# Performance work log

Hardware: AMD Instinct MI355X
Metric: run time of the kernel (lower is better)

Reference implementation:

```python
import jax, jax.numpy as jnp
import numpy as np

N, IN_F, OUT_F, R = 8192, 4096, 4096, 16
ALPHA = 32
SCALING = ALPHA / R  # 2.0


def setup_inputs() -> dict:
    key = jax.random.key(0)
    k1, k2, k3, k4, k5 = jax.random.split(key, 5)
    return {
        "x": jax.random.normal(k1, (N, IN_F), dtype=jnp.float32),
        "W": jax.random.normal(k2, (OUT_F, IN_F), dtype=jnp.float32) * 0.02,
        "b": jax.random.normal(k3, (OUT_F,), dtype=jnp.float32) * 0.02,
        "lora_A": jax.random.normal(k4, (R, IN_F), dtype=jnp.float32) * 0.02,
        "lora_B": jax.random.normal(k5, (OUT_F, R), dtype=jnp.float32) * 0.02,
    }


def reference(x, W, b, lora_A, lora_B):
    # Base linear: x [N, in_f] @ W.T [in_f, out_f] + b -> [N, out_f]
    result = jnp.einsum('ni,oi->no', x, W) + b
    # LoRA path: (B @ (A @ x.T)).T * scaling == (x @ A.T) @ B.T * scaling
    lora = jnp.einsum('nr,or->no', jnp.einsum('ni,ri->nr', x, lora_A), lora_B)
    return result + lora * SCALING
```

## Files before the change

### kernel.cpp

```cpp
#include <hip/hip_runtime.h>
#include <hip/hip_bf16.h>
#include <stdint.h>

#define N_ROWS 8192
#define IN_F   4096
#define OUT_F  4096
#define R_LORA 16
#define KP     4160

typedef __bf16 bf16_t;
typedef __attribute__((ext_vector_type(8))) __bf16 bf16x8;
typedef __attribute__((ext_vector_type(4))) __bf16 bf16x4;
typedef __attribute__((ext_vector_type(4))) float  f32x4;

__device__ __forceinline__ void load16_lds(const bf16_t* g, bf16_t* l) {
    auto gp = (const __attribute__((address_space(1))) void*)g;
    auto lp = (__attribute__((address_space(3))) void*)(uint32_t)(uintptr_t)l;
    __builtin_amdgcn_global_load_lds(gp, lp, 16, 0, 0);
}

__global__ __launch_bounds__(256) void prep_a(const float* __restrict__ x,
                                              bf16_t* __restrict__ Aw) {
    int row = blockIdx.x;
    const float4* xr = (const float4*)(x + (size_t)row * IN_F);
    bf16_t* ar = Aw + (size_t)row * KP;
    int t = threadIdx.x;
    for (int s = t; s < 512; s += 256) {
        float4 f0 = xr[2 * s];
        float4 f1 = xr[2 * s + 1];
        bf16x8 v;
        v[0] = (bf16_t)f0.x; v[1] = (bf16_t)f0.y;
        v[2] = (bf16_t)f0.z; v[3] = (bf16_t)f0.w;
        v[4] = (bf16_t)f1.x; v[5] = (bf16_t)f1.y;
        v[6] = (bf16_t)f1.z; v[7] = (bf16_t)f1.w;
        *(bf16x8*)(ar + s * 8) = v;
    }
    if (t < 64) ar[IN_F + t] = (t == 0) ? (bf16_t)1.0f : (bf16_t)0.0f;
}

__global__ __launch_bounds__(256) void prep_b(const float* __restrict__ W,
                                              const float* __restrict__ bias,
                                              const float* __restrict__ lA,
                                              const float* __restrict__ lB,
                                              bf16_t* __restrict__ Bw) {
    int o0 = blockIdx.x * 4;
    int t  = threadIdx.x;

    float bl[4][R_LORA];
    for (int oo = 0; oo < 4; ++oo)
        for (int r = 0; r < R_LORA; ++r)
            bl[oo][r] = 2.0f * lB[(o0 + oo) * R_LORA + r];

    for (int j = 0; j < IN_F / (256 * 4); ++j) {
        int i4 = (j * 256 + t) * 4;
        f32x4 acc[4];
        for (int oo = 0; oo < 4; ++oo) {
            float4 w = *(const float4*)(W + (size_t)(o0 + oo) * IN_F + i4);
            acc[oo] = (f32x4){w.x, w.y, w.z, w.w};
        }
        for (int r = 0; r < R_LORA; ++r) {
            float4 a = *(const float4*)(lA + (size_t)r * IN_F + i4);
            for (int oo = 0; oo < 4; ++oo) {
                acc[oo][0] += bl[oo][r] * a.x;
                acc[oo][1] += bl[oo][r] * a.y;
                acc[oo][2] += bl[oo][r] * a.z;
                acc[oo][3] += bl[oo][r] * a.w;
            }
        }
        for (int oo = 0; oo < 4; ++oo) {
            bf16x4 v;
            v[0] = (bf16_t)acc[oo][0]; v[1] = (bf16_t)acc[oo][1];
            v[2] = (bf16_t)acc[oo][2]; v[3] = (bf16_t)acc[oo][3];
            *(bf16x4*)(Bw + (size_t)(o0 + oo) * KP + i4) = v;
        }
    }
    {
        int oo = t >> 6;
        int c  = IN_F + (t & 63);
        float v = (c == IN_F) ? bias[o0 + oo] : 0.0f;
        Bw[(size_t)(o0 + oo) * KP + c] = (bf16_t)v;
    }
}

#define BM 128
#define BN 128
#define BK 64

__global__ __launch_bounds__(256) void gemm_bt(const bf16_t* __restrict__ A,
                                               const bf16_t* __restrict__ B,
                                               float* __restrict__ C) {
    __shared__ bf16_t As[BM * BK];
    __shared__ bf16_t Bs[BN * BK];

    int bid = blockIdx.x;
    int bn  = bid & 31;
    int bm  = bid >> 5;
    int rowBase = bm * BM;
    int colBase = bn * BN;

    int t    = threadIdx.x;
    int lane = t & 63;
    int wave = t >> 6;
    int wr   = wave >> 1, wc = wave & 1;
    int quad = lane >> 4;
    int ln15 = lane & 15;
    int l7   = ln15 & 7;

    f32x4 acc[4][4];
    for (int i = 0; i < 4; ++i)
        for (int j = 0; j < 4; ++j) acc[i][j] = (f32x4){0.f, 0.f, 0.f, 0.f};

    const int kIters = KP / BK;

    for (int kt = 0; kt < kIters; ++kt) {
        int k0 = kt * BK;
        for (int i = 0; i < 4; ++i) {
            int slot = i * 256 + t;
            int r  = slot >> 3;
            int p  = slot & 7;
            int srcOff = ((p ^ (r & 7)) * 8);
            load16_lds(A + (size_t)(rowBase + r) * KP + k0 + srcOff, &As[slot * 8]);
            load16_lds(B + (size_t)(colBase + r) * KP + k0 + srcOff, &Bs[slot * 8]);
        }
        __syncthreads();

        for (int kk = 0; kk < BK; kk += 32) {
            int cb = kk >> 3;
            int posOff = ((cb + quad) ^ l7) * 8;
            bf16x8 af[4], bfr[4];
            for (int mi = 0; mi < 4; ++mi) {
                int row = wr * 64 + mi * 16 + ln15;
                af[mi] = *(const bf16x8*)&As[row * BK + posOff];
            }
            for (int ni = 0; ni < 4; ++ni) {
                int col = wc * 64 + ni * 16 + ln15;
                bfr[ni] = *(const bf16x8*)&Bs[col * BK + posOff];
            }
            for (int mi = 0; mi < 4; ++mi)
                for (int ni = 0; ni < 4; ++ni)
                    acc[mi][ni] = __builtin_amdgcn_mfma_f32_16x16x32_bf16(
                        af[mi], bfr[ni], acc[mi][ni], 0, 0, 0);
        }
        __syncthreads();
    }

    for (int mi = 0; mi < 4; ++mi) {
        int row0 = rowBase + wr * 64 + mi * 16 + quad * 4;
        for (int ni = 0; ni < 4; ++ni) {
            int col = colBase + wc * 64 + ni * 16 + ln15;
            for (int reg = 0; reg < 4; ++reg)
                C[(size_t)(row0 + reg) * OUT_F + col] = acc[mi][ni][reg];
        }
    }
}

extern "C" void kernel_launch(void* const* d_in, const int* in_sizes, int n_in,
                              void* d_out, int out_size, void* d_ws, size_t ws_size,
                              hipStream_t stream) {
    const float* x  = (const float*)d_in[0];
    const float* W  = (const float*)d_in[1];
    const float* b  = (const float*)d_in[2];
    const float* lA = (const float*)d_in[3];
    const float* lB = (const float*)d_in[4];
    float* out = (float*)d_out;

    bf16_t* Aw = (bf16_t*)d_ws;
    bf16_t* Bw = Aw + (size_t)N_ROWS * KP;

    prep_a<<<N_ROWS, 256, 0, stream>>>(x, Aw);
    prep_b<<<OUT_F / 4, 256, 0, stream>>>(W, b, lA, lB, Bw);
    gemm_bt<<<(N_ROWS / BM) * (OUT_F / BN), 256, 0, stream>>>(Aw, Bw, out);
}
```

Measured before the change: 625.4 us.

## Fuse prep kernels into one launch and switch GEMM to 32x32x16 MFMA

The two preprocessing kernels are merged into one launch. Its first 2048 blocks each convert four rows of x to bf16, and the remaining blocks build the folded W+LoRA+bias matrix. This removes a launch and lets both jobs share the GPU. The GEMM inner loop now uses 32x32x16 bf16 MFMA tiles instead of 16x16x32, cutting the number of MFMA issues and LDS fragment loads per K step. The LDS swizzle indexing and the output store mapping are reworked to match, which risks mismatches in the fragment layout.

Measured after the change: 557.7 us. 1.12x faster.

```diff
diff --git a/kernel.cpp b/kernel.cpp
--- a/kernel.cpp
+++ b/kernel.cpp
@@ -12,6 +12,7 @@
 typedef __attribute__((ext_vector_type(8))) __bf16 bf16x8;
 typedef __attribute__((ext_vector_type(4))) __bf16 bf16x4;
 typedef __attribute__((ext_vector_type(4))) float  f32x4;
+typedef __attribute__((ext_vector_type(16))) float f32x16;
 
 __device__ __forceinline__ void load16_lds(const bf16_t* g, bf16_t* l) {
     auto gp = (const __attribute__((address_space(1))) void*)g;
@@ -19,66 +20,71 @@
     __builtin_amdgcn_global_load_lds(gp, lp, 16, 0, 0);
 }
 
-__global__ __launch_bounds__(256) void prep_a(const float* __restrict__ x,
-                                              bf16_t* __restrict__ Aw) {
-    int row = blockIdx.x;
-    const float4* xr = (const float4*)(x + (size_t)row * IN_F);
-    bf16_t* ar = Aw + (size_t)row * KP;
+#define PREPA_BLOCKS 2048
+
+__global__ __launch_bounds__(256) void prep_fused(const float* __restrict__ x,
+                                                  const float* __restrict__ W,
+                                                  const float* __restrict__ bias,
+                                                  const float* __restrict__ lA,
+                                                  const float* __restrict__ lB,
+                                                  bf16_t* __restrict__ Aw,
+                                                  bf16_t* __restrict__ Bw) {
+    int b = blockIdx.x;
     int t = threadIdx.x;
-    for (int s = t; s < 512; s += 256) {
-        float4 f0 = xr[2 * s];
-        float4 f1 = xr[2 * s + 1];
-        bf16x8 v;
-        v[0] = (bf16_t)f0.x; v[1] = (bf16_t)f0.y;
-        v[2] = (bf16_t)f0.z; v[3] = (bf16_t)f0.w;
-        v[4] = (bf16_t)f1.x; v[5] = (bf16_t)f1.y;
-        v[6] = (bf16_t)f1.z; v[7] = (bf16_t)f1.w;
-        *(bf16x8*)(ar + s * 8) = v;
-    }
-    if (t < 64) ar[IN_F + t] = (t == 0) ? (bf16_t)1.0f : (bf16_t)0.0f;
-}
+    if (b < PREPA_BLOCKS) {
+        int row0 = b * 4;
+        for (int rr = 0; rr < 4; ++rr) {
+            int row = row0 + rr;
+            const float4* xr = (const float4*)(x + (size_t)row * IN_F);
+            bf16_t* ar = Aw + (size_t)row * KP;
+            for (int s = t; s < 512; s += 256) {
+                float4 f0 = xr[2 * s];
+                float4 f1 = xr[2 * s + 1];
+                bf16x8 v;
+                v[0] = (bf16_t)f0.x; v[1] = (bf16_t)f0.y;
+                v[2] = (bf16_t)f0.z; v[3] = (bf16_t)f0.w;
+                v[4] = (bf16_t)f1.x; v[5] = (bf16_t)f1.y;
+                v[6] = (bf16_t)f1.z; v[7] = (bf16_t)f1.w;
+                *(bf16x8*)(ar + s * 8) = v;
+            }
+            if (t < 64) ar[IN_F + t] = (t == 0) ? (bf16_t)1.0f : (bf16_t)0.0f;
+        }
+    } else {
+        int o0 = (b - PREPA_BLOCKS) * 4;
+        float bl[4][R_LORA];
+        for (int oo = 0; oo < 4; ++oo)
+            for (int r = 0; r < R_LORA; ++r)
+                bl[oo][r] = 2.0f * lB[(o0 + oo) * R_LORA + r];
 
-__global__ __launch_bounds__(256) void prep_b(const float* __restrict__ W,
-                                              const float* __restrict__ bias,
-                                              const float* __restrict__ lA,
-                                              const float* __restrict__ lB,
-                                              bf16_t* __restrict__ Bw) {
-    int o0 = blockIdx.x * 4;
-    int t  = threadIdx.x;
-
-    float bl[4][R_LORA];
-    for (int oo = 0; oo < 4; ++oo)
-        for (int r = 0; r < R_LORA; ++r)
-            bl[oo][r] = 2.0f * lB[(o0 + oo) * R_LORA + r];
-
-    for (int j = 0; j < IN_F / (256 * 4); ++j) {
-        int i4 = (j * 256 + t) * 4;
-        f32x4 acc[4];
-        for (int oo = 0; oo < 4; ++oo) {
-            float4 w = *(const float4*)(W + (size_t)(o0 + oo) * IN_F + i4);
-            acc[oo] = (f32x4){w.x, w.y, w.z, w.w};
-        }
-        for (int r = 0; r < R_LORA; ++r) {
-            float4 a = *(const float4*)(lA + (size_t)r * IN_F + i4);
+        for (int j = 0; j < IN_F / (256 * 4); ++j) {
+            int i4 = (j * 256 + t) * 4;
+            f32x4 acc[4];
             for (int oo = 0; oo < 4; ++oo) {
-                acc[oo][0] += bl[oo][r] * a.x;
-                acc[oo][1] += bl[oo][r] * a.y;
-                acc[oo][2] += bl[oo][r] * a.z;
-                acc[oo][3] += bl[oo][r] * a.w;
+                float4 w = *(const float4*)(W + (size_t)(o0 + oo) * IN_F + i4);
+                acc[oo] = (f32x4){w.x, w.y, w.z, w.w};
+            }
+            for (int r = 0; r < R_LORA; ++r) {
+                float4 a = *(const float4*)(lA + (size_t)r * IN_F + i4);
+                for (int oo = 0; oo < 4; ++oo) {
+                    acc[oo][0] += bl[oo][r] * a.x;
+                    acc[oo][1] += bl[oo][r] * a.y;
+                    acc[oo][2] += bl[oo][r] * a.z;
+                    acc[oo][3] += bl[oo][r] * a.w;
+                }
+            }
+            for (int oo = 0; oo < 4; ++oo) {
+                bf16x4 v;
+                v[0] = (bf16_t)acc[oo][0]; v[1] = (bf16_t)acc[oo][1];
+                v[2] = (bf16_t)acc[oo][2]; v[3] = (bf16_t)acc[oo][3];
+                *(bf16x4*)(Bw + (size_t)(o0 + oo) * KP + i4) = v;
             }
         }
-        for (int oo = 0; oo < 4; ++oo) {
-            bf16x4 v;
-            v[0] = (bf16_t)acc[oo][0]; v[1] = (bf16_t)acc[oo][1];
-            v[2] = (bf16_t)acc[oo][2]; v[3] = (bf16_t)acc[oo][3];
-            *(bf16x4*)(Bw + (size_t)(o0 + oo) * KP + i4) = v;
+        {
+            int oo = t >> 6;
+            int c  = IN_F + (t & 63);
+            float v = (c == IN_F) ? bias[o0 + oo] : 0.0f;
+            Bw[(size_t)(o0 + oo) * KP + c] = (bf16_t)v;
         }
-    }
-    {
-        int oo = t >> 6;
-        int c  = IN_F + (t & 63);
-        float v = (c == IN_F) ? bias[o0 + oo] : 0.0f;
-        Bw[(size_t)(o0 + oo) * KP + c] = (bf16_t)v;
     }
 }
 
@@ -102,13 +108,14 @@
     int lane = t & 63;
     int wave = t >> 6;
     int wr   = wave >> 1, wc = wave & 1;
-    int quad = lane >> 4;
-    int ln15 = lane & 15;
-    int l7   = ln15 & 7;
+    int l31  = lane & 31;
+    int lhi  = lane >> 5;
+    int l7   = lane & 7;
 
-    f32x4 acc[4][4];
-    for (int i = 0; i < 4; ++i)
-        for (int j = 0; j < 4; ++j) acc[i][j] = (f32x4){0.f, 0.f, 0.f, 0.f};
+    f32x16 acc[2][2];
+    for (int i = 0; i < 2; ++i)
+        for (int j = 0; j < 2; ++j)
+            for (int r = 0; r < 16; ++r) acc[i][j][r] = 0.f;
 
     const int kIters = KP / BK;
 
@@ -124,32 +131,34 @@
         }
         __syncthreads();
 
-        for (int kk = 0; kk < BK; kk += 32) {
-            int cb = kk >> 3;
-            int posOff = ((cb + quad) ^ l7) * 8;
-            bf16x8 af[4], bfr[4];
-            for (int mi = 0; mi < 4; ++mi) {
-                int row = wr * 64 + mi * 16 + ln15;
-                af[mi] = *(const bf16x8*)&As[row * BK + posOff];
+        for (int ks = 0; ks < 4; ++ks) {
+            int chunk = (ks << 1) + lhi;
+            int posOff = (chunk ^ l7) * 8;
+            bf16x8 af[2], bfg[2];
+            for (int ti = 0; ti < 2; ++ti) {
+                int row = wr * 64 + ti * 32 + l31;
+                af[ti] = *(const bf16x8*)&As[row * BK + posOff];
             }
-            for (int ni = 0; ni < 4; ++ni) {
-                int col = wc * 64 + ni * 16 + ln15;
-                bfr[ni] = *(const bf16x8*)&Bs[col * BK + posOff];
+            for (int tj = 0; tj < 2; ++tj) {
+                int col = wc * 64 + tj * 32 + l31;
+                bfg[tj] = *(const bf16x8*)&Bs[col * BK + posOff];
             }
-            for (int mi = 0; mi < 4; ++mi)
-                for (int ni = 0; ni < 4; ++ni)
-                    acc[mi][ni] = __builtin_amdgcn_mfma_f32_16x16x32_bf16(
-                        af[mi], bfr[ni], acc[mi][ni], 0, 0, 0);
+            for (int ti = 0; ti < 2; ++ti)
+                for (int tj = 0; tj < 2; ++tj)
+                    acc[ti][tj] = __builtin_amdgcn_mfma_f32_32x32x16_bf16(
+                        af[ti], bfg[tj], acc[ti][tj], 0, 0, 0);
         }
         __syncthreads();
     }
 
-    for (int mi = 0; mi < 4; ++mi) {
-        int row0 = rowBase + wr * 64 + mi * 16 + quad * 4;
-        for (int ni = 0; ni < 4; ++ni) {
-            int col = colBase + wc * 64 + ni * 16 + ln15;
-            for (int reg = 0; reg < 4; ++reg)
-                C[(size_t)(row0 + reg) * OUT_F + col] = acc[mi][ni][reg];
+    for (int ti = 0; ti < 2; ++ti) {
+        int rB = rowBase + wr * 64 + ti * 32 + 4 * lhi;
+        for (int tj = 0; tj < 2; ++tj) {
+            int col = colBase + wc * 64 + tj * 32 + l31;
+            for (int reg = 0; reg < 16; ++reg) {
+                int row = rB + (reg & 3) + 8 * (reg >> 2);
+                C[(size_t)row * OUT_F + col] = acc[ti][tj][reg];
+            }
         }
     }
 }
@@ -167,7 +176,6 @@
     bf16_t* Aw = (bf16_t*)d_ws;
     bf16_t* Bw = Aw + (size_t)N_ROWS * KP;
 
-    prep_a<<<N_ROWS, 256, 0, stream>>>(x, Aw);
-    prep_b<<<OUT_F / 4, 256, 0, stream>>>(W, b, lA, lB, Bw);
+    prep_fused<<<PREPA_BLOCKS + OUT_F / 4, 256, 0, stream>>>(x, W, b, lA, lB, Aw, Bw);
     gemm_bt<<<(N_ROWS / BM) * (OUT_F / BN), 256, 0, stream>>>(Aw, Bw, out);
 }
```
